# Optimization experiments

Measured on AMD Instinct MI355X. Metric: run time of the kernel, lower is better.

## Reference

```python
import jax, jax.numpy as jnp
import numpy as np

N_NODES = 100000
N_EDGES = 3200000
NEG_SLOPE = 0.2  # PyG GATConv default


def _gat_conv(x, src, dst, W, a_src, a_dst, b, num_nodes):
    # x: [N, Fin]; src/dst: [E'] (self-loops already appended)
    h = x @ W                                   # [N, Fout]
    alpha_src = h @ a_src                       # [N]
    alpha_dst = h @ a_dst                       # [N]
    e = jax.nn.leaky_relu(alpha_src[src] + alpha_dst[dst], NEG_SLOPE)  # [E']
    # segment softmax over incoming edges of each destination node
    e_max = jax.ops.segment_max(e, dst, num_segments=num_nodes)
    e_exp = jnp.exp(e - e_max[dst])
    denom = jax.ops.segment_sum(e_exp, dst, num_segments=num_nodes)
    alpha = e_exp / (denom[dst] + 1e-16)        # [E']
    out = jax.ops.segment_sum(h[src] * alpha[:, None], dst, num_segments=num_nodes)
    return out + b


def setup_inputs() -> dict:
    key = jax.random.key(0)
    ks = jax.random.split(key, 10)
    x = jax.random.normal(ks[0], (N_NODES, 1), jnp.float32)
    edge_index = jax.random.randint(ks[1], (2, N_EDGES), 0, N_NODES, dtype=jnp.int64)
    s1 = 1.0  # glorot-ish scales
    return {
        "x": x,
        "edge_index": edge_index,
        "W1": jax.random.normal(ks[2], (1, 20), jnp.float32) * s1,
        "a_src1": jax.random.normal(ks[3], (20,), jnp.float32) * 0.3,
        "a_dst1": jax.random.normal(ks[4], (20,), jnp.float32) * 0.3,
        "b1": jnp.zeros((20,), jnp.float32),
        "W2": jax.random.normal(ks[5], (20, 20), jnp.float32) * (1.0 / np.sqrt(20.0)),
        "a_src2": jax.random.normal(ks[6], (20,), jnp.float32) * 0.3,
        "a_dst2": jax.random.normal(ks[7], (20,), jnp.float32) * 0.3,
        "b2": jnp.zeros((20,), jnp.float32),
        "Wl": jax.random.normal(ks[8], (20, 1), jnp.float32) * (1.0 / np.sqrt(20.0)),
        "bl": jnp.zeros((1,), jnp.float32),
    }


def reference(x, edge_index, W1, a_src1, a_dst1, b1, W2, a_src2, a_dst2, b2, Wl, bl):
    n = x.shape[0]
    loop = jnp.arange(n, dtype=edge_index.dtype)
    src = jnp.concatenate([edge_index[0], loop])  # add_self_loops=True
    dst = jnp.concatenate([edge_index[1], loop])
    h = _gat_conv(x, src, dst, W1, a_src1, a_dst1, b1, n)
    h = jax.nn.relu(h)
    h = _gat_conv(h, src, dst, W2, a_src2, a_dst2, b2, n)
    h = jax.nn.relu(h)
    return h @ Wl + bl  # [N, 1]
```

## Files before the change

### kernel.cpp

```cpp
#include <hip/hip_runtime.h>
#include <hip/hip_fp16.h>

#define FDIM 20
#define NSLOPE 0.2f
#define BSHIFT 7
#define BSIZE 128
#define BCAP 4800
#define MAXBUCK 800
#define PGRID 256
#define HSTRIDE 32

__device__ __forceinline__ float lrelu(float v) { return v > 0.f ? v : NSLOPE * v; }

__global__ void k_init(const float* __restrict__ x, const float* __restrict__ W1,
                       const float* __restrict__ a_src, const float* __restrict__ a_dst,
                       float2* __restrict__ PX, float* __restrict__ AD,
                       int* __restrict__ gcur, int N)
{
    int i = blockIdx.x * blockDim.x + threadIdx.x;
    if (i < MAXBUCK) gcur[i] = 0;
    if (i >= N) return;
    float cs = 0.f, cd = 0.f;
#pragma unroll
    for (int f = 0; f < FDIM; ++f) { float w = W1[f]; cs += w * a_src[f]; cd += w * a_dst[f]; }
    float xv = x[i];
    PX[i] = make_float2(xv * cs, xv);
    AD[i] = xv * cd;
}

__global__ void __launch_bounds__(1024)
k_part(const int* __restrict__ ei, int E, int nbuck,
       int* __restrict__ gcur, int* __restrict__ slab)
{
    __shared__ int hist[MAXBUCK];
    __shared__ int base[MAXBUCK];
    const int chunk = (E + PGRID - 1) / PGRID;
    const int c0 = blockIdx.x * chunk;
    const int c1 = min(c0 + chunk, E);
    for (int t = threadIdx.x; t < nbuck; t += blockDim.x) hist[t] = 0;
    __syncthreads();
    for (int i = c0 + threadIdx.x; i < c1; i += blockDim.x)
        atomicAdd(&hist[ei[E + i] >> BSHIFT], 1);
    __syncthreads();
    for (int t = threadIdx.x; t < nbuck; t += blockDim.x) {
        int c = hist[t];
        base[t] = c ? atomicAdd(gcur + t, c) : 0;
        hist[t] = 0;
    }
    __syncthreads();
    for (int i = c0 + threadIdx.x; i < c1; i += blockDim.x) {
        int s = ei[i], d = ei[E + i];
        int b = d >> BSHIFT;
        int lp = atomicAdd(&hist[b], 1);
        int pos = base[b] + lp;
        if (pos < BCAP)
            slab[(size_t)b * BCAP + pos] = (s << BSHIFT) | (d & (BSIZE - 1));
    }
}

__device__ __forceinline__ void sort_bucket(const int* __restrict__ sp, int cnt,
                                            int* __restrict__ sedge,
                                            int* __restrict__ off,
                                            int* __restrict__ cur)
{
    const int tid = threadIdx.x;
    if (tid < BSIZE + 1) off[tid] = 0;
    __syncthreads();
    for (int i = tid; i < cnt; i += 256)
        atomicAdd(&off[(sp[i] & (BSIZE - 1)) + 1], 1);
    __syncthreads();
    for (int o = 1; o < BSIZE; o <<= 1) {
        int v = 0;
        if (tid < BSIZE && tid + 1 > o) v = off[tid + 1 - o];
        __syncthreads();
        if (tid < BSIZE) off[tid + 1] += v;
        __syncthreads();
    }
    if (tid < BSIZE) cur[tid] = off[tid];
    __syncthreads();
    for (int i = tid; i < cnt; i += 256) {
        int e = sp[i];
        int pos = atomicAdd(&cur[e & (BSIZE - 1)], 1);
        sedge[pos] = e >> BSHIFT;
    }
    __syncthreads();
}

__global__ void __launch_bounds__(256)
k_agg1(const int* __restrict__ gcur, const int* __restrict__ slab,
       const float2* __restrict__ PX, const float* __restrict__ AD,
       const float* __restrict__ W1, const float* __restrict__ b1,
       const float* __restrict__ W2,
       const float* __restrict__ as2w, const float* __restrict__ ad2w,
       __half* __restrict__ H, float* __restrict__ AD2, int N)
{
    __shared__ int sedge[BCAP];
    __shared__ int off[BSIZE + 1], cur[BSIZE];
    __shared__ float sAD[BSIZE];
    __shared__ float sW1[FDIM], sb1[FDIM], sW2[FDIM * FDIM], sas[FDIM], sad[FDIM];
    const int tid = threadIdx.x;
    const int b = blockIdx.x;
    const int dbase = b << BSHIFT;
    if (tid < BSIZE) { int d = dbase + tid; sAD[tid] = (d < N) ? AD[d] : 0.f; }
    for (int t = tid; t < FDIM * FDIM; t += 256) sW2[t] = W2[t];
    if (tid >= 224 && tid < 224 + FDIM) {
        int k = tid - 224;
        sW1[k] = W1[k]; sb1[k] = b1[k]; sas[k] = as2w[k]; sad[k] = ad2w[k];
    }
    const int cnt = min(gcur[b], BCAP);
    sort_bucket(slab + (size_t)b * BCAP, cnt, sedge, off, cur);

    const int dl = tid >> 1, sub = tid & 1;
    const float adv = sAD[dl];
    float den = 0.f, sx = 0.f;
    const int e1 = off[dl + 1];
#pragma unroll 2
    for (int j = off[dl] + sub; j < e1; j += 2) {
        int s = sedge[j];
        float2 p = PX[s];
        float w = __expf(lrelu(p.x + adv));
        den += w; sx += w * p.y;
    }
    den += __shfl_xor(den, 1);
    sx  += __shfl_xor(sx, 1);
    const int d = dbase + dl;
    if (sub == 0 && d < N) {
        float2 p = PX[d];
        float w = __expf(lrelu(p.x + adv));
        den += w; sx += w * p.y;
        float sv = sx / (den + 1e-16f);
        float tk[FDIM];
#pragma unroll
        for (int k = 0; k < FDIM; ++k) {
            float tv = sv * sW1[k] + sb1[k];
            tk[k] = tv > 0.f ? tv : 0.f;
        }
        float pas = 0.f, pad = 0.f;
        __half2* hrow = (__half2*)(H + (size_t)d * HSTRIDE);
#pragma unroll
        for (int f = 0; f < FDIM; f += 2) {
            float h0 = 0.f, h1 = 0.f;
#pragma unroll
            for (int k = 0; k < FDIM; ++k) {
                h0 += tk[k] * sW2[k * FDIM + f];
                h1 += tk[k] * sW2[k * FDIM + f + 1];
            }
            hrow[f >> 1] = __halves2half2(__float2half(h0), __float2half(h1));
            pas += h0 * sas[f] + h1 * sas[f + 1];
            pad += h0 * sad[f] + h1 * sad[f + 1];
        }
        *(float*)(H + (size_t)d * HSTRIDE + FDIM) = pas;
        AD2[d] = pad;
    }
}

__global__ void __launch_bounds__(256)
k_agg2(const int* __restrict__ gcur, const int* __restrict__ slab,
       const __half* __restrict__ H, const float* __restrict__ AD2,
       const float* __restrict__ b2, const float* __restrict__ Wl,
       const float* __restrict__ bl,
       float* __restrict__ out, int N)
{
    __shared__ int sedge[BCAP];
    __shared__ int off[BSIZE + 1], cur[BSIZE];
    __shared__ float sAD[BSIZE];
    __shared__ float sb2[FDIM], sWl[FDIM];
    const int tid = threadIdx.x;
    const int b = blockIdx.x;
    const int dbase = b << BSHIFT;
    if (tid < BSIZE) { int d = dbase + tid; sAD[tid] = (d < N) ? AD2[d] : 0.f; }
    if (tid >= 224 && tid < 224 + FDIM) {
        int k = tid - 224;
        sb2[k] = b2[k]; sWl[k] = Wl[k];
    }
    const int cnt = min(gcur[b], BCAP);
    sort_bucket(slab + (size_t)b * BCAP, cnt, sedge, off, cur);

    const int dl = tid >> 1, sub = tid & 1;
    const float adv = sAD[dl];
    float den = 0.f;
    float acc[FDIM];
#pragma unroll
    for (int k = 0; k < FDIM; ++k) acc[k] = 0.f;
    const int e1 = off[dl + 1];
#pragma unroll 2
    for (int j = off[dl] + sub; j < e1; j += 2) {
        int s = sedge[j];
        const uint4* rp = (const uint4*)(H + (size_t)s * HSTRIDE);
        uint4 a = rp[0];
        uint4 bb = rp[1];
        uint4 c = rp[2];
        float w = __expf(lrelu(__uint_as_float(c.z) + adv));
        den += w;
        float2 f;
        f = __half22float2(*(__half2*)&a.x);  acc[0]  += w * f.x; acc[1]  += w * f.y;
        f = __half22float2(*(__half2*)&a.y);  acc[2]  += w * f.x; acc[3]  += w * f.y;
        f = __half22float2(*(__half2*)&a.z);  acc[4]  += w * f.x; acc[5]  += w * f.y;
        f = __half22float2(*(__half2*)&a.w);  acc[6]  += w * f.x; acc[7]  += w * f.y;
        f = __half22float2(*(__half2*)&bb.x); acc[8]  += w * f.x; acc[9]  += w * f.y;
        f = __half22float2(*(__half2*)&bb.y); acc[10] += w * f.x; acc[11] += w * f.y;
        f = __half22float2(*(__half2*)&bb.z); acc[12] += w * f.x; acc[13] += w * f.y;
        f = __half22float2(*(__half2*)&bb.w); acc[14] += w * f.x; acc[15] += w * f.y;
        f = __half22float2(*(__half2*)&c.x);  acc[16] += w * f.x; acc[17] += w * f.y;
        f = __half22float2(*(__half2*)&c.y);  acc[18] += w * f.x; acc[19] += w * f.y;
    }
    den += __shfl_xor(den, 1);
#pragma unroll
    for (int k = 0; k < FDIM; ++k) acc[k] += __shfl_xor(acc[k], 1);
    const int d = dbase + dl;
    if (sub == 0 && d < N) {
        const uint4* rp = (const uint4*)(H + (size_t)d * HSTRIDE);
        uint4 a = rp[0], bb = rp[1], c = rp[2];
        float w = __expf(lrelu(__uint_as_float(c.z) + adv));
        den += w;
        float hv[FDIM];
        float2 f;
        f = __half22float2(*(__half2*)&a.x);  hv[0]  = f.x; hv[1]  = f.y;
        f = __half22float2(*(__half2*)&a.y);  hv[2]  = f.x; hv[3]  = f.y;
        f = __half22float2(*(__half2*)&a.z);  hv[4]  = f.x; hv[5]  = f.y;
        f = __half22float2(*(__half2*)&a.w);  hv[6]  = f.x; hv[7]  = f.y;
        f = __half22float2(*(__half2*)&bb.x); hv[8]  = f.x; hv[9]  = f.y;
        f = __half22float2(*(__half2*)&bb.y); hv[10] = f.x; hv[11] = f.y;
        f = __half22float2(*(__half2*)&bb.z); hv[12] = f.x; hv[13] = f.y;
        f = __half22float2(*(__half2*)&bb.w); hv[14] = f.x; hv[15] = f.y;
        f = __half22float2(*(__half2*)&c.x);  hv[16] = f.x; hv[17] = f.y;
        f = __half22float2(*(__half2*)&c.y);  hv[18] = f.x; hv[19] = f.y;
        float inv = 1.f / (den + 1e-16f);
        float r = 0.f;
#pragma unroll
        for (int k = 0; k < FDIM; ++k) {
            float v = (acc[k] + w * hv[k]) * inv + sb2[k];
            v = v > 0.f ? v : 0.f;
            r += v * sWl[k];
        }
        out[d] = r + bl[0];
    }
}

extern "C" void kernel_launch(void* const* d_in, const int* in_sizes, int n_in,
                              void* d_out, int out_size, void* d_ws, size_t ws_size,
                              hipStream_t stream)
{
    const float* x      = (const float*)d_in[0];
    const int*   ei     = (const int*)d_in[1];
    const float* W1     = (const float*)d_in[2];
    const float* a_src1 = (const float*)d_in[3];
    const float* a_dst1 = (const float*)d_in[4];
    const float* b1     = (const float*)d_in[5];
    const float* W2     = (const float*)d_in[6];
    const float* a_src2 = (const float*)d_in[7];
    const float* a_dst2 = (const float*)d_in[8];
    const float* b2     = (const float*)d_in[9];
    const float* Wl     = (const float*)d_in[10];
    const float* bl     = (const float*)d_in[11];
    float* out = (float*)d_out;

    const int N = in_sizes[0];
    const int E = in_sizes[1] / 2;
    const int NBUCK = (N + BSIZE - 1) >> BSHIFT;

    __half* H   = (__half*)d_ws;
    float2* PX  = (float2*)(H + (size_t)N * HSTRIDE);
    float*  AD  = (float*)(PX + N);
    float*  AD2 = AD + N;
    int*  gcur  = (int*)(AD2 + N);
    int*  slab  = gcur + MAXBUCK;

    const int nb_n = (N + 255) / 256;

    k_init<<<nb_n, 256, 0, stream>>>(x, W1, a_src1, a_dst1, PX, AD, gcur, N);
    k_part<<<PGRID, 1024, 0, stream>>>(ei, E, NBUCK, gcur, slab);
    k_agg1<<<NBUCK, 256, 0, stream>>>(gcur, slab, PX, AD, W1, b1, W2,
                                      a_src2, a_dst2, H, AD2, N);
    k_agg2<<<NBUCK, 256, 0, stream>>>(gcur, slab, H, AD2, b2, Wl, bl, out, N);
}
```

Measured before the change: 203.6 us.

## Use four lanes per destination node in aggregation and vectorize partition loads

The aggregation kernels now launch 512 threads per bucket, so each destination node is handled by four lanes instead of two, and partial sums are combined with a two-step xor shuffle. The bucket sort loops now stride by blockDim. The partition kernel reads edge indices as int2 pairs to halve the number of load instructions. The goal is more memory-level parallelism for the gather-heavy edge loops, at the cost of an extra shuffle round and larger blocks that may limit how many blocks fit per CU.

```diff
diff --git a/kernel.cpp b/kernel.cpp
--- a/kernel.cpp
+++ b/kernel.cpp
@@ -9,6 +9,7 @@
 #define MAXBUCK 800
 #define PGRID 256
 #define HSTRIDE 32
+#define ABLK 512
 
 __device__ __forceinline__ float lrelu(float v) { return v > 0.f ? v : NSLOPE * v; }
 
@@ -37,24 +38,40 @@
     const int chunk = (E + PGRID - 1) / PGRID;
     const int c0 = blockIdx.x * chunk;
     const int c1 = min(c0 + chunk, E);
-    for (int t = threadIdx.x; t < nbuck; t += blockDim.x) hist[t] = 0;
-    __syncthreads();
-    for (int i = c0 + threadIdx.x; i < c1; i += blockDim.x)
-        atomicAdd(&hist[ei[E + i] >> BSHIFT], 1);
-    __syncthreads();
-    for (int t = threadIdx.x; t < nbuck; t += blockDim.x) {
+    for (int t = threadIdx.x; t < nbuck; t += 1024) hist[t] = 0;
+    __syncthreads();
+    int i = c0 + 2 * threadIdx.x;
+    for (; i + 1 < c1; i += 2048) {
+        int2 d2 = *(const int2*)(ei + E + i);
+        atomicAdd(&hist[d2.x >> BSHIFT], 1);
+        atomicAdd(&hist[d2.y >> BSHIFT], 1);
+    }
+    if (i < c1) atomicAdd(&hist[ei[E + i] >> BSHIFT], 1);
+    __syncthreads();
+    for (int t = threadIdx.x; t < nbuck; t += 1024) {
         int c = hist[t];
         base[t] = c ? atomicAdd(gcur + t, c) : 0;
         hist[t] = 0;
     }
     __syncthreads();
-    for (int i = c0 + threadIdx.x; i < c1; i += blockDim.x) {
+    i = c0 + 2 * threadIdx.x;
+    for (; i + 1 < c1; i += 2048) {
+        int2 s2 = *(const int2*)(ei + i);
+        int2 d2 = *(const int2*)(ei + E + i);
+        int bA = d2.x >> BSHIFT, bB = d2.y >> BSHIFT;
+        int lpA = atomicAdd(&hist[bA], 1);
+        int lpB = atomicAdd(&hist[bB], 1);
+        int pA = base[bA] + lpA;
+        int pB = base[bB] + lpB;
+        if (pA < BCAP) slab[(size_t)bA * BCAP + pA] = (s2.x << BSHIFT) | (d2.x & (BSIZE - 1));
+        if (pB < BCAP) slab[(size_t)bB * BCAP + pB] = (s2.y << BSHIFT) | (d2.y & (BSIZE - 1));
+    }
+    if (i < c1) {
         int s = ei[i], d = ei[E + i];
         int b = d >> BSHIFT;
         int lp = atomicAdd(&hist[b], 1);
         int pos = base[b] + lp;
-        if (pos < BCAP)
-            slab[(size_t)b * BCAP + pos] = (s << BSHIFT) | (d & (BSIZE - 1));
+        if (pos < BCAP) slab[(size_t)b * BCAP + pos] = (s << BSHIFT) | (d & (BSIZE - 1));
     }
 }
 
@@ -66,7 +83,7 @@
     const int tid = threadIdx.x;
     if (tid < BSIZE + 1) off[tid] = 0;
     __syncthreads();
-    for (int i = tid; i < cnt; i += 256)
+    for (int i = tid; i < cnt; i += blockDim.x)
         atomicAdd(&off[(sp[i] & (BSIZE - 1)) + 1], 1);
     __syncthreads();
     for (int o = 1; o < BSIZE; o <<= 1) {
@@ -78,7 +95,7 @@
     }
     if (tid < BSIZE) cur[tid] = off[tid];
     __syncthreads();
-    for (int i = tid; i < cnt; i += 256) {
+    for (int i = tid; i < cnt; i += blockDim.x) {
         int e = sp[i];
         int pos = atomicAdd(&cur[e & (BSIZE - 1)], 1);
         sedge[pos] = e >> BSHIFT;
@@ -86,7 +103,7 @@
     __syncthreads();
 }
 
-__global__ void __launch_bounds__(256)
+__global__ void __launch_bounds__(ABLK)
 k_agg1(const int* __restrict__ gcur, const int* __restrict__ slab,
        const float2* __restrict__ PX, const float* __restrict__ AD,
        const float* __restrict__ W1, const float* __restrict__ b1,
@@ -102,27 +119,27 @@
     const int b = blockIdx.x;
     const int dbase = b << BSHIFT;
     if (tid < BSIZE) { int d = dbase + tid; sAD[tid] = (d < N) ? AD[d] : 0.f; }
-    for (int t = tid; t < FDIM * FDIM; t += 256) sW2[t] = W2[t];
-    if (tid >= 224 && tid < 224 + FDIM) {
-        int k = tid - 224;
+    for (int t = tid; t < FDIM * FDIM; t += ABLK) sW2[t] = W2[t];
+    if (tid >= 480 && tid < 480 + FDIM) {
+        int k = tid - 480;
         sW1[k] = W1[k]; sb1[k] = b1[k]; sas[k] = as2w[k]; sad[k] = ad2w[k];
     }
     const int cnt = min(gcur[b], BCAP);
     sort_bucket(slab + (size_t)b * BCAP, cnt, sedge, off, cur);
 
-    const int dl = tid >> 1, sub = tid & 1;
+    const int dl = tid >> 2, sub = tid & 3;
     const float adv = sAD[dl];
     float den = 0.f, sx = 0.f;
     const int e1 = off[dl + 1];
 #pragma unroll 2
-    for (int j = off[dl] + sub; j < e1; j += 2) {
+    for (int j = off[dl] + sub; j < e1; j += 4) {
         int s = sedge[j];
         float2 p = PX[s];
         float w = __expf(lrelu(p.x + adv));
         den += w; sx += w * p.y;
     }
-    den += __shfl_xor(den, 1);
-    sx  += __shfl_xor(sx, 1);
+    den += __shfl_xor(den, 1); den += __shfl_xor(den, 2);
+    sx  += __shfl_xor(sx, 1);  sx  += __shfl_xor(sx, 2);
     const int d = dbase + dl;
     if (sub == 0 && d < N) {
         float2 p = PX[d];
@@ -154,7 +171,7 @@
     }
 }
 
-__global__ void __launch_bounds__(256)
+__global__ void __launch_bounds__(ABLK)
 k_agg2(const int* __restrict__ gcur, const int* __restrict__ slab,
        const __half* __restrict__ H, const float* __restrict__ AD2,
        const float* __restrict__ b2, const float* __restrict__ Wl,
@@ -169,14 +186,14 @@
     const int b = blockIdx.x;
     const int dbase = b << BSHIFT;
     if (tid < BSIZE) { int d = dbase + tid; sAD[tid] = (d < N) ? AD2[d] : 0.f; }
-    if (tid >= 224 && tid < 224 + FDIM) {
-        int k = tid - 224;
+    if (tid >= 480 && tid < 480 + FDIM) {
+        int k = tid - 480;
         sb2[k] = b2[k]; sWl[k] = Wl[k];
     }
     const int cnt = min(gcur[b], BCAP);
     sort_bucket(slab + (size_t)b * BCAP, cnt, sedge, off, cur);
 
-    const int dl = tid >> 1, sub = tid & 1;
+    const int dl = tid >> 2, sub = tid & 3;
     const float adv = sAD[dl];
     float den = 0.f;
     float acc[FDIM];
@@ -184,7 +201,7 @@
     for (int k = 0; k < FDIM; ++k) acc[k] = 0.f;
     const int e1 = off[dl + 1];
 #pragma unroll 2
-    for (int j = off[dl] + sub; j < e1; j += 2) {
+    for (int j = off[dl] + sub; j < e1; j += 4) {
         int s = sedge[j];
         const uint4* rp = (const uint4*)(H + (size_t)s * HSTRIDE);
         uint4 a = rp[0];
@@ -204,9 +221,12 @@
         f = __half22float2(*(__half2*)&c.x);  acc[16] += w * f.x; acc[17] += w * f.y;
         f = __half22float2(*(__half2*)&c.y);  acc[18] += w * f.x; acc[19] += w * f.y;
     }
-    den += __shfl_xor(den, 1);
-#pragma unroll
-    for (int k = 0; k < FDIM; ++k) acc[k] += __shfl_xor(acc[k], 1);
+    den += __shfl_xor(den, 1); den += __shfl_xor(den, 2);
+#pragma unroll
+    for (int k = 0; k < FDIM; ++k) {
+        acc[k] += __shfl_xor(acc[k], 1);
+        acc[k] += __shfl_xor(acc[k], 2);
+    }
     const int d = dbase + dl;
     if (sub == 0 && d < N) {
         const uint4* rp = (const uint4*)(H + (size_t)d * HSTRIDE);
@@ -270,7 +290,7 @@
 
     k_init<<<nb_n, 256, 0, stream>>>(x, W1, a_src1, a_dst1, PX, AD, gcur, N);
     k_part<<<PGRID, 1024, 0, stream>>>(ei, E, NBUCK, gcur, slab);
-    k_agg1<<<NBUCK, 256, 0, stream>>>(gcur, slab, PX, AD, W1, b1, W2,
-                                      a_src2, a_dst2, H, AD2, N);
-    k_agg2<<<NBUCK, 256, 0, stream>>>(gcur, slab, H, AD2, b2, Wl, bl, out, N);
-}
+    k_agg1<<<NBUCK, ABLK, 0, stream>>>(gcur, slab, PX, AD, W1, b1, W2,
+                                       a_src2, a_dst2, H, AD2, N);
+    k_agg2<<<NBUCK, ABLK, 0, stream>>>(gcur, slab, H, AD2, b2, Wl, bl, out, N);
+}
```

Result: faster. 195.3 us (-4.1%).
